# Optimization experiments

Hardware: AMD Instinct MI355X
Metric: run time of the kernel (lower is better)

The kernel has to match this reference:

```python
import jax, jax.numpy as jnp
import numpy as np

B, S, H = 4, 512, 128

def setup_inputs() -> dict:
    key = jax.random.key(0)
    k_inp, k_m, k_w0, k_b0, k_w1, k_b1 = jax.random.split(key, 6)
    inp = jax.random.normal(k_inp, (B, S, H), dtype=jnp.float32)
    masks = jax.random.randint(k_m, (B, S), 0, 2, dtype=jnp.int32)
    # nn.Linear params: weight [out,in], bias [out]
    lim = 1.0 / np.sqrt(H)
    W0 = jax.random.uniform(k_w0, (H, H), jnp.float32, -lim, lim)
    b0 = jax.random.uniform(k_b0, (H,), jnp.float32, -lim, lim)
    W1 = jax.random.uniform(k_w1, (H, H), jnp.float32, -lim, lim)
    b1 = jax.random.uniform(k_b1, (H,), jnp.float32, -lim, lim)
    return {"inp": inp, "masks": masks, "W0": W0, "b0": b0, "W1": W1, "b1": b1}

def reference(inp, masks, W0, b0, W1, b1):
    # inp: [B,S,H], masks: [B,S] int {0,1}
    mf = masks.astype(inp.dtype)
    sentence_lengths = jnp.sum(mf, axis=1)                      # [B]
    gate_0 = jnp.einsum('bsh,oh->bso', inp, W0) + b0            # [B,S,H]
    gate_1 = jnp.einsum('bsh,oh->bso', inp, W1) + b1            # [B,S,H]
    # pairwise broadcast gate: [B,S(i),S(j),H]
    forget_gate = jax.nn.sigmoid(gate_0[:, :, None, :] + gate_1[:, None, :, :])
    # gate the row-expanded input (inp indexed by j)
    forget_result = inp[:, None, :, :] * forget_gate            # [B,S,S,H]
    pair_mask = mf[:, :, None] * mf[:, None, :]                 # [B,S,S]
    context_sumup = jnp.sum(forget_result * pair_mask[:, :, :, None], axis=2)  # [B,S,H]
    context_vector = context_sumup / sentence_lengths[:, None, None]
    return jnp.tanh(context_vector)
```

## Files before the change

kernel.cpp:

```cpp
#include <hip/hip_runtime.h>
#include <hip/hip_bf16.h>


#define BB 4
#define SS 512
#define HH 128
#define R1 4

__global__ __launch_bounds__(256) void kA(const float* __restrict__ inp,
                                          const int* __restrict__ masks,
                                          const float* __restrict__ W0,
                                          const float* __restrict__ b0,
                                          const float* __restrict__ W1,
                                          const float* __restrict__ b1,
                                          float* __restrict__ E0,
                                          float2* __restrict__ XE,
                                          int* __restrict__ valid_idx,
                                          int* __restrict__ nvalid,
                                          float* __restrict__ rcpL,
                                          float* __restrict__ out) {
    if (blockIdx.x == (BB * SS) / R1) {
        int wave = threadIdx.x >> 6, lane = threadIdx.x & 63;
        if (wave >= BB) return;
        int b = wave, base = 0;
        for (int c = 0; c < SS; c += 64) {
            int m = masks[b * SS + c + lane];
            unsigned long long bits = __ballot(m != 0);
            int pos = __popcll(bits & ((1ull << lane) - 1ull));
            if (m) valid_idx[b * SS + base + pos] = c + lane;
            base += __popcll(bits);
        }
        if (lane == 0) {
            nvalid[b] = base;
            rcpL[b] = base ? 1.0f / (float)base : 0.0f;
        }
        return;
    }

    __shared__ float s_inp[R1][HH];
    const int row0 = blockIdx.x * R1;
    const int tid = threadIdx.x;

    if (tid < 128) {
        const float4* src = (const float4*)(inp + (size_t)row0 * HH);
        float4* dst = (float4*)&s_inp[0][0];
        dst[tid] = src[tid];
    }
    __syncthreads();

    const int o = tid & 127;
    const int g = tid >> 7;
    const float* __restrict__ W = g ? W1 : W0;
    const float bias = g ? b1[o] : b0[o];

    float acc[R1];
#pragma unroll
    for (int r = 0; r < R1; ++r) acc[r] = bias;

    const float* __restrict__ Wrow = W + (size_t)o * HH;
#pragma unroll 4
    for (int k = 0; k < HH; k += 4) {
        float4 w4 = *(const float4*)(Wrow + k);
#pragma unroll
        for (int r = 0; r < R1; ++r) {
            float4 x4 = *(const float4*)&s_inp[r][k];
            float a = acc[r];
            a = fmaf(x4.x, w4.x, a);
            a = fmaf(x4.y, w4.y, a);
            a = fmaf(x4.z, w4.z, a);
            a = fmaf(x4.w, w4.w, a);
            acc[r] = a;
        }
    }

    if (g == 0) {
#pragma unroll
        for (int r = 0; r < R1; ++r)
            E0[(size_t)(row0 + r) * HH + o] =
                __builtin_amdgcn_exp2f(acc[r] * 1.44269504088896f);
#pragma unroll
        for (int r = 0; r < R1; ++r)
            if (masks[row0 + r] == 0) out[(size_t)(row0 + r) * HH + o] = 0.0f;
    } else {
#pragma unroll
        for (int r = 0; r < R1; ++r) {
            float e1 = __builtin_amdgcn_exp2f(acc[r] * 1.44269504088896f);
            XE[(size_t)(row0 + r) * HH + o] = make_float2(s_inp[r][o], e1);
        }
    }
}

__global__ __launch_bounds__(1024) void kB(const float* __restrict__ E0,
                                           const float2* __restrict__ XE,
                                           const int* __restrict__ valid_idx,
                                           const int* __restrict__ nvalid,
                                           const float* __restrict__ rcpL,
                                           float* __restrict__ out) {
    const int b = blockIdx.x >> 7;
    const int qi = blockIdx.x & 127;
    const int nv = nvalid[b];
    const int p0 = qi * 4;
    if (p0 >= nv) return;

    __shared__ float red[8][4][HH];
    __shared__ int s_vj[SS];

    const int tid = threadIdx.x;
    const int h = tid & 127;
    const int oc = tid >> 7;

    if (tid < nv) s_vj[tid] = valid_idx[b * SS + tid];
    __syncthreads();

    const size_t boff = (size_t)b * SS * HH;
    const float* __restrict__ E0b = E0 + boff;
    const float2* __restrict__ XEb = XE + boff;

    float e0r[4];
#pragma unroll
    for (int r = 0; r < 4; ++r)
        e0r[r] = (p0 + r < nv) ? E0b[(size_t)s_vj[p0 + r] * HH + h] : 0.0f;

    const int chunk = (nv + 7) >> 3;
    const int jb = oc * chunk;
    const int je = min(nv, jb + chunk);

    float acc[4] = {0.f, 0.f, 0.f, 0.f};
    float sumx = 0.f;
#pragma unroll 4
    for (int t = jb; t < je; ++t) {
        const int j = s_vj[t];
        const float2 v = XEb[(size_t)j * HH + h];
        const float x = v.x, e1 = v.y;
        sumx += x;
#pragma unroll
        for (int r = 0; r < 4; ++r) {
            const float t0 = e0r[r] * e1;
            acc[r] = fmaf(x, __builtin_amdgcn_rcpf(1.0f + t0), acc[r]);
        }
    }

#pragma unroll
    for (int r = 0; r < 4; ++r) red[oc][r][h] = sumx - acc[r];
    __syncthreads();

    if (tid < 512) {
        const int r = tid >> 7;
        if (p0 + r < nv) {
            const int hh = tid & 127;
            float s = 0.f;
#pragma unroll
            for (int q = 0; q < 8; ++q) s += red[q][r][hh];
            float x = s * rcpL[b];
            x = fminf(fmaxf(x, -30.0f), 30.0f);
            const float e = __builtin_amdgcn_exp2f(x * 2.885390081777927f);
            const float th = (e - 1.0f) * __builtin_amdgcn_rcpf(e + 1.0f);
            out[boff + (size_t)s_vj[p0 + r] * HH + hh] = th;
        }
    }
}

extern "C" void kernel_launch(void* const* d_in, const int* in_sizes, int n_in,
                              void* d_out, int out_size, void* d_ws, size_t ws_size,
                              hipStream_t stream) {
    const float* inp = (const float*)d_in[0];
    const int* masks = (const int*)d_in[1];
    const float* W0 = (const float*)d_in[2];
    const float* b0 = (const float*)d_in[3];
    const float* W1 = (const float*)d_in[4];
    const float* b1 = (const float*)d_in[5];
    float* out = (float*)d_out;

    const size_t nBSH = (size_t)BB * SS * HH;
    float* E0 = (float*)d_ws;
    float2* XE = (float2*)(E0 + nBSH);
    int* valid_idx = (int*)(XE + nBSH);
    int* nvalid = valid_idx + BB * SS;
    float* rcpL = (float*)(nvalid + BB);

    kA<<<(BB * SS) / R1 + 1, 256, 0, stream>>>(inp, masks, W0, b0, W1, b1,
                                               E0, XE, valid_idx, nvalid, rcpL, out);
    kB<<<BB * (SS / 4), 1024, 0, stream>>>(E0, XE, valid_idx, nvalid, rcpL, out);
}
```

Baseline: 28.02 us.

## Transpose weights in a prep kernel, double rows per block, simplify sigmoid math

Adds a prep kernel that transposes W0/W1 so the projection kernel reads weights coalesced across output lanes, and moves mask compaction into it. The projection kernel now handles 8 rows per block, reads inputs directly (broadcast) without shared memory, and stores exp(-g1) instead of exp(g1). The pairwise kernel then uses x*re1 * rcp(re1+e0) to save one multiply per inner iteration. This costs an extra kernel launch and a weight transpose pass on every call.

```diff
diff --git a/kernel.cpp b/kernel.cpp
--- a/kernel.cpp
+++ b/kernel.cpp
@@ -5,21 +5,17 @@
 #define BB 4
 #define SS 512
 #define HH 128
-#define R1 4
+#define RA 8
+#define L2E 1.44269504088896f
 
-__global__ __launch_bounds__(256) void kA(const float* __restrict__ inp,
-                                          const int* __restrict__ masks,
-                                          const float* __restrict__ W0,
-                                          const float* __restrict__ b0,
-                                          const float* __restrict__ W1,
-                                          const float* __restrict__ b1,
-                                          float* __restrict__ E0,
-                                          float2* __restrict__ XE,
-                                          int* __restrict__ valid_idx,
-                                          int* __restrict__ nvalid,
-                                          float* __restrict__ rcpL,
-                                          float* __restrict__ out) {
-    if (blockIdx.x == (BB * SS) / R1) {
+__global__ __launch_bounds__(256) void k_prep(const float* __restrict__ W0,
+                                              const float* __restrict__ W1,
+                                              const int* __restrict__ masks,
+                                              float* __restrict__ WT,
+                                              int* __restrict__ valid_idx,
+                                              int* __restrict__ nvalid,
+                                              float* __restrict__ rcpL) {
+    if (blockIdx.x == 32) {
         int wave = threadIdx.x >> 6, lane = threadIdx.x & 63;
         if (wave >= BB) return;
         int b = wave, base = 0;
@@ -36,56 +32,60 @@
         }
         return;
     }
+    const int flat = blockIdx.x * 256 + threadIdx.x;
+    const int g = flat >> 12;
+    const int rem = flat & 4095;
+    const int k4 = rem >> 7;
+    const int o = rem & 127;
+    const float* __restrict__ W = g ? W1 : W0;
+    float4 w = *(const float4*)(W + (size_t)o * HH + k4 * 4);
+    float* __restrict__ WTg = WT + (size_t)g * HH * HH;
+    WTg[(size_t)(k4 * 4 + 0) * HH + o] = w.x;
+    WTg[(size_t)(k4 * 4 + 1) * HH + o] = w.y;
+    WTg[(size_t)(k4 * 4 + 2) * HH + o] = w.z;
+    WTg[(size_t)(k4 * 4 + 3) * HH + o] = w.w;
+}
 
-    __shared__ float s_inp[R1][HH];
-    const int row0 = blockIdx.x * R1;
-    const int tid = threadIdx.x;
+__global__ __launch_bounds__(256) void kA(const float* __restrict__ inp,
+                                          const int* __restrict__ masks,
+                                          const float* __restrict__ WT,
+                                          const float* __restrict__ b0,
+                                          const float* __restrict__ b1,
+                                          float* __restrict__ E0,
+                                          float2* __restrict__ XE,
+                                          float* __restrict__ out) {
+    const int row0 = blockIdx.x * RA;
+    const int o = threadIdx.x & 127;
+    const int g = threadIdx.x >> 7;
+    const float bias = g ? b1[o] : b0[o];
+    const float* __restrict__ WTg = WT + (size_t)g * HH * HH;
+    const float* __restrict__ xbase = inp + (size_t)row0 * HH;
 
-    if (tid < 128) {
-        const float4* src = (const float4*)(inp + (size_t)row0 * HH);
-        float4* dst = (float4*)&s_inp[0][0];
-        dst[tid] = src[tid];
-    }
-    __syncthreads();
+    float acc[RA];
+#pragma unroll
+    for (int r = 0; r < RA; ++r) acc[r] = bias;
 
-    const int o = tid & 127;
-    const int g = tid >> 7;
-    const float* __restrict__ W = g ? W1 : W0;
-    const float bias = g ? b1[o] : b0[o];
-
-    float acc[R1];
+#pragma unroll 8
+    for (int k = 0; k < HH; ++k) {
+        const float w = WTg[(size_t)k * HH + o];
 #pragma unroll
-    for (int r = 0; r < R1; ++r) acc[r] = bias;
-
-    const float* __restrict__ Wrow = W + (size_t)o * HH;
-#pragma unroll 4
-    for (int k = 0; k < HH; k += 4) {
-        float4 w4 = *(const float4*)(Wrow + k);
-#pragma unroll
-        for (int r = 0; r < R1; ++r) {
-            float4 x4 = *(const float4*)&s_inp[r][k];
-            float a = acc[r];
-            a = fmaf(x4.x, w4.x, a);
-            a = fmaf(x4.y, w4.y, a);
-            a = fmaf(x4.z, w4.z, a);
-            a = fmaf(x4.w, w4.w, a);
-            acc[r] = a;
-        }
+        for (int r = 0; r < RA; ++r)
+            acc[r] = fmaf(xbase[(size_t)r * HH + k], w, acc[r]);
     }
 
     if (g == 0) {
 #pragma unroll
-        for (int r = 0; r < R1; ++r)
-            E0[(size_t)(row0 + r) * HH + o] =
-                __builtin_amdgcn_exp2f(acc[r] * 1.44269504088896f);
+        for (int r = 0; r < RA; ++r)
+            E0[(size_t)(row0 + r) * HH + o] = __builtin_amdgcn_exp2f(acc[r] * L2E);
 #pragma unroll
-        for (int r = 0; r < R1; ++r)
+        for (int r = 0; r < RA; ++r)
             if (masks[row0 + r] == 0) out[(size_t)(row0 + r) * HH + o] = 0.0f;
     } else {
 #pragma unroll
-        for (int r = 0; r < R1; ++r) {
-            float e1 = __builtin_amdgcn_exp2f(acc[r] * 1.44269504088896f);
-            XE[(size_t)(row0 + r) * HH + o] = make_float2(s_inp[r][o], e1);
+        for (int r = 0; r < RA; ++r) {
+            const float re1 = __builtin_amdgcn_exp2f(-acc[r] * L2E);
+            const float x = inp[(size_t)(row0 + r) * HH + o];
+            XE[(size_t)(row0 + r) * HH + o] = make_float2(x, re1);
         }
     }
 }
@@ -131,13 +131,12 @@
     for (int t = jb; t < je; ++t) {
         const int j = s_vj[t];
         const float2 v = XEb[(size_t)j * HH + h];
-        const float x = v.x, e1 = v.y;
+        const float x = v.x, re1 = v.y;
         sumx += x;
+        const float xr = x * re1;
 #pragma unroll
-        for (int r = 0; r < 4; ++r) {
-            const float t0 = e0r[r] * e1;
-            acc[r] = fmaf(x, __builtin_amdgcn_rcpf(1.0f + t0), acc[r]);
-        }
+        for (int r = 0; r < 4; ++r)
+            acc[r] = fmaf(xr, __builtin_amdgcn_rcpf(re1 + e0r[r]), acc[r]);
     }
 
 #pragma unroll
@@ -174,11 +173,12 @@
     const size_t nBSH = (size_t)BB * SS * HH;
     float* E0 = (float*)d_ws;
     float2* XE = (float2*)(E0 + nBSH);
-    int* valid_idx = (int*)(XE + nBSH);
+    float* WT = (float*)(XE + nBSH);
+    int* valid_idx = (int*)(WT + 2 * HH * HH);
     int* nvalid = valid_idx + BB * SS;
     float* rcpL = (float*)(nvalid + BB);
 
-    kA<<<(BB * SS) / R1 + 1, 256, 0, stream>>>(inp, masks, W0, b0, W1, b1,
-                                               E0, XE, valid_idx, nvalid, rcpL, out);
+    k_prep<<<33, 256, 0, stream>>>(W0, W1, masks, WT, valid_idx, nvalid, rcpL);
+    kA<<<(BB * SS) / RA, 256, 0, stream>>>(inp, masks, WT, b0, b1, E0, XE, out);
     kB<<<BB * (SS / 4), 1024, 0, stream>>>(E0, XE, valid_idx, nvalid, rcpL, out);
 }
```

After: 31.84 us. 1.14x slower.

## Stage weights in swizzled LDS per gate and fold one multiply out of pair loop

Applied to the files above, without the earlier changes.

Kernel A now splits blocks by gate and row group: each block loads its full 128x128 weight matrix into XOR-swizzled shared memory and reads the input rows straight from global memory. Kernel B's inner loop is rewritten algebraically: storing exp(-g1) instead of exp(g1) lets x/(1+e0*e1) become x*exp(-g1)/(exp(-g1)+e0), so the per-pair multiply moves out of the r loop. The kernel B unroll factor is also raised from 4 to 8. Staging 64KB of weights per block raises LDS traffic and lowers occupancy in exchange for fewer scattered global weight reads.

```diff
diff --git a/kernel.cpp b/kernel.cpp
--- a/kernel.cpp
+++ b/kernel.cpp
@@ -5,7 +5,8 @@
 #define BB 4
 #define SS 512
 #define HH 128
-#define R1 4
+#define RA 8
+#define L2E 1.44269504088896f
 
 __global__ __launch_bounds__(256) void kA(const float* __restrict__ inp,
                                           const int* __restrict__ masks,
@@ -19,7 +20,8 @@
                                           int* __restrict__ nvalid,
                                           float* __restrict__ rcpL,
                                           float* __restrict__ out) {
-    if (blockIdx.x == (BB * SS) / R1) {
+    const int bid = blockIdx.x;
+    if (bid == 512) {
         int wave = threadIdx.x >> 6, lane = threadIdx.x & 63;
         if (wave >= BB) return;
         int b = wave, base = 0;
@@ -37,55 +39,57 @@
         return;
     }
 
-    __shared__ float s_inp[R1][HH];
-    const int row0 = blockIdx.x * R1;
-    const int tid = threadIdx.x;
+    __shared__ float4 sW[32 * 128];
 
-    if (tid < 128) {
-        const float4* src = (const float4*)(inp + (size_t)row0 * HH);
-        float4* dst = (float4*)&s_inp[0][0];
-        dst[tid] = src[tid];
+    const int g = bid & 1;
+    const int row0 = (bid >> 1) * RA;
+    const float* __restrict__ W = g ? W1 : W0;
+
+#pragma unroll
+    for (int it = 0; it < 16; ++it) {
+        const int flat = it * 256 + threadIdx.x;
+        const int q = flat & 31;
+        const int o = flat >> 5;
+        const float4 w = *(const float4*)(W + (size_t)o * HH + q * 4);
+        sW[q * 128 + (o ^ q)] = w;
     }
     __syncthreads();
 
-    const int o = tid & 127;
-    const int g = tid >> 7;
-    const float* __restrict__ W = g ? W1 : W0;
+    const int o = threadIdx.x & 127;
+    const int rh = threadIdx.x >> 7;
+    const int r0 = row0 + rh * 4;
+    const float* __restrict__ xb = inp + (size_t)r0 * HH;
     const float bias = g ? b1[o] : b0[o];
 
-    float acc[R1];
+    float acc[4] = {bias, bias, bias, bias};
+#pragma unroll 4
+    for (int q = 0; q < 32; ++q) {
+        const float4 w = sW[q * 128 + (o ^ q)];
 #pragma unroll
-    for (int r = 0; r < R1; ++r) acc[r] = bias;
-
-    const float* __restrict__ Wrow = W + (size_t)o * HH;
-#pragma unroll 4
-    for (int k = 0; k < HH; k += 4) {
-        float4 w4 = *(const float4*)(Wrow + k);
-#pragma unroll
-        for (int r = 0; r < R1; ++r) {
-            float4 x4 = *(const float4*)&s_inp[r][k];
+        for (int r = 0; r < 4; ++r) {
+            const float4 x = *(const float4*)(xb + (size_t)r * HH + q * 4);
             float a = acc[r];
-            a = fmaf(x4.x, w4.x, a);
-            a = fmaf(x4.y, w4.y, a);
-            a = fmaf(x4.z, w4.z, a);
-            a = fmaf(x4.w, w4.w, a);
+            a = fmaf(x.x, w.x, a);
+            a = fmaf(x.y, w.y, a);
+            a = fmaf(x.z, w.z, a);
+            a = fmaf(x.w, w.w, a);
             acc[r] = a;
         }
     }
 
     if (g == 0) {
 #pragma unroll
-        for (int r = 0; r < R1; ++r)
-            E0[(size_t)(row0 + r) * HH + o] =
-                __builtin_amdgcn_exp2f(acc[r] * 1.44269504088896f);
+        for (int r = 0; r < 4; ++r)
+            E0[(size_t)(r0 + r) * HH + o] = __builtin_amdgcn_exp2f(acc[r] * L2E);
 #pragma unroll
-        for (int r = 0; r < R1; ++r)
-            if (masks[row0 + r] == 0) out[(size_t)(row0 + r) * HH + o] = 0.0f;
+        for (int r = 0; r < 4; ++r)
+            if (masks[r0 + r] == 0) out[(size_t)(r0 + r) * HH + o] = 0.0f;
     } else {
 #pragma unroll
-        for (int r = 0; r < R1; ++r) {
-            float e1 = __builtin_amdgcn_exp2f(acc[r] * 1.44269504088896f);
-            XE[(size_t)(row0 + r) * HH + o] = make_float2(s_inp[r][o], e1);
+        for (int r = 0; r < 4; ++r) {
+            const float re1 = __builtin_amdgcn_exp2f(-acc[r] * L2E);
+            const float x = inp[(size_t)(r0 + r) * HH + o];
+            XE[(size_t)(r0 + r) * HH + o] = make_float2(x, re1);
         }
     }
 }
@@ -127,17 +131,16 @@
 
     float acc[4] = {0.f, 0.f, 0.f, 0.f};
     float sumx = 0.f;
-#pragma unroll 4
+#pragma unroll 8
     for (int t = jb; t < je; ++t) {
         const int j = s_vj[t];
         const float2 v = XEb[(size_t)j * HH + h];
-        const float x = v.x, e1 = v.y;
+        const float x = v.x, re1 = v.y;
         sumx += x;
+        const float xr = x * re1;
 #pragma unroll
-        for (int r = 0; r < 4; ++r) {
-            const float t0 = e0r[r] * e1;
-            acc[r] = fmaf(x, __builtin_amdgcn_rcpf(1.0f + t0), acc[r]);
-        }
+        for (int r = 0; r < 4; ++r)
+            acc[r] = fmaf(xr, __builtin_amdgcn_rcpf(re1 + e0r[r]), acc[r]);
     }
 
 #pragma unroll
@@ -178,7 +181,7 @@
     int* nvalid = valid_idx + BB * SS;
     float* rcpL = (float*)(nvalid + BB);
 
-    kA<<<(BB * SS) / R1 + 1, 256, 0, stream>>>(inp, masks, W0, b0, W1, b1,
-                                               E0, XE, valid_idx, nvalid, rcpL, out);
+    kA<<<513, 256, 0, stream>>>(inp, masks, W0, b0, W1, b1,
+                                E0, XE, valid_idx, nvalid, rcpL, out);
     kB<<<BB * (SS / 4), 1024, 0, stream>>>(E0, XE, valid_idx, nvalid, rcpL, out);
 }
```

After: 30.64 us. 9.3% more time.
